# Optimization experiments

Measured on AMD Instinct MI355X. Metric: run time of the kernel, lower is better.

## Reference

```python
import jax, jax.numpy as jnp
import numpy as np

B, NB, H, E, NCT, NL = 16, 4096, 128, 65536, 32, 2
LN_EPS = 1e-5


def _layernorm(x, scale, bias):
    mu = jnp.mean(x, axis=-1, keepdims=True)
    var = jnp.var(x, axis=-1, keepdims=True)
    return (x - mu) / jnp.sqrt(var + LN_EPS) * scale + bias


def setup_inputs() -> dict:
    key = jax.random.key(0)
    ks = jax.random.split(key, 18)
    s = 1.0 / np.sqrt(H)
    inp = {
        'block_tokens': jax.random.normal(ks[0], (B, NB, H), jnp.float32),
        'edge_structure': jnp.full((E,), 0.5, jnp.float32),
        'ct_emb': 0.1 * jax.random.normal(ks[1], (NCT, E), jnp.float32),
        'W_proj': s * jax.random.normal(ks[2], (H, H), jnp.float32),
        'b_proj': jnp.zeros((H,), jnp.float32),
        'W_gate': (1.0 / np.sqrt(2 * H)) * jax.random.normal(ks[3], (2 * H, H), jnp.float32),
        'b_gate': jnp.zeros((H,), jnp.float32),
        'ln_scale': jnp.ones((NL, H), jnp.float32),
        'ln_bias': jnp.zeros((NL, H), jnp.float32),
        'W1': s * jax.random.normal(ks[4], (NL, H, 2 * H), jnp.float32),
        'b1': jnp.zeros((NL, 2 * H), jnp.float32),
        'W2': (1.0 / np.sqrt(2 * H)) * jax.random.normal(ks[5], (NL, 2 * H, H), jnp.float32),
        'b2': jnp.zeros((NL, H), jnp.float32),
        'cancer_type': jax.random.randint(ks[6], (B,), 0, NCT),
        'edge_src': jax.random.randint(ks[7], (E,), 0, NB),
        'edge_dst': jax.random.randint(ks[8], (E,), 0, NB),
        'block_active': jax.random.bernoulli(ks[9], 0.9, (B, NB)),
    }
    return inp


def reference(block_tokens, edge_structure, ct_emb, W_proj, b_proj, W_gate, b_gate,
              ln_scale, ln_bias, W1, b1, W2, b2,
              cancer_type, edge_src, edge_dst, block_active):
    # per-edge signed weights, masked by active src/dst blocks  -> (B, E)
    structure = jax.nn.sigmoid(edge_structure)
    edge_w = structure[None, :] * ct_emb[cancer_type]
    edge_w = edge_w * block_active[:, edge_src].astype(edge_w.dtype) \
                    * block_active[:, edge_dst].astype(edge_w.dtype)
    # route projection + ELU
    h_route = jax.nn.elu(jnp.einsum('bnh,hd->bnd', block_tokens, W_proj) + b_proj)
    # gather sources, weight, scatter-add to destinations
    weighted = edge_w[..., None] * h_route[:, edge_src, :]          # (B, E, H)
    messages = jnp.zeros_like(block_tokens).at[:, edge_dst, :].add(weighted)
    # gated residual
    gate = jax.nn.sigmoid(
        jnp.einsum('bnh,hd->bnd', jnp.concatenate([block_tokens, messages], axis=-1), W_gate) + b_gate)
    x = block_tokens + gate * messages
    # norm + FFN layers (dropout is identity at inference)
    for l in range(NL):
        normed = _layernorm(x, ln_scale[l], ln_bias[l])
        h = jax.nn.elu(jnp.einsum('bnh,hf->bnf', normed, W1[l]) + b1[l])
        x = x + jnp.einsum('bnf,fh->bnh', h, W2[l]) + b2[l]
    return (x, edge_w)
```

## Files before the change

kernel.cpp:

```cpp
#include <hip/hip_runtime.h>
#include <hip/hip_bf16.h>

#define BB     16
#define NBLK   4096
#define HD     128
#define NE     65536
#define MTOT   (BB * NBLK)

typedef __attribute__((ext_vector_type(8))) short bf16x8;
typedef __attribute__((ext_vector_type(4))) float f32x4;

__device__ __forceinline__ float bf2f(unsigned short u) {
    union { unsigned int i; float f; } v; v.i = ((unsigned int)u) << 16; return v.f;
}
__device__ __forceinline__ unsigned short f2bf(float f) {
    union { float f; unsigned int i; } v; v.f = f;
    unsigned int u = v.i;
    unsigned int r = u + 0x7FFFu + ((u >> 16) & 1u);
    return (unsigned short)(r >> 16);
}
__device__ __forceinline__ float ldf(const void* p, size_t i, int f32m) {
    return f32m ? ((const float*)p)[i] : bf2f(((const unsigned short*)p)[i]);
}
__device__ __forceinline__ int get_active(const void* p, int i, int mode) {
    switch (mode) {
        case 1:  return ((const unsigned char*)p)[i] != 0;
        case 2:  return ((const unsigned short*)p)[i] != 0;
        case 3:  return ((const float*)p)[i] != 0.f;
        default: return ((const int*)p)[i] != 0;
    }
}
__device__ __forceinline__ float elu_f(float v) {
    const float e = __expf(v);
    return v > 0.f ? v : e - 1.f;
}
__device__ __forceinline__ float sig_f(float v) {
    return 1.f / (1.f + __expf(-v));
}

__global__ void probe_k(const unsigned int* __restrict__ es,
                        const unsigned int* __restrict__ act,
                        int* __restrict__ flags)
{
    const int lane = threadIdx.x;
    const unsigned int v0 = act[lane], v1 = act[64 + lane];
    auto le1  = [](unsigned int v) { return v <= 1u; };
    auto byt  = [](unsigned int v) {
        return ((v & 0xFFu) <= 1u) && (((v >> 8) & 0xFFu) <= 1u) &&
               (((v >> 16) & 0xFFu) <= 1u) && ((v >> 24) <= 1u); };
    auto f32b = [](unsigned int v) { return v == 0u || v == 0x3F800000u; };
    auto bfb  = [](unsigned int v) {
        unsigned short h0 = (unsigned short)(v & 0xFFFFu), h1 = (unsigned short)(v >> 16);
        return (h0 == 0u || h0 == 0x3F80u) && (h1 == 0u || h1 == 0x3F80u); };
    const unsigned long long m_le1 = __ballot(le1(v0) && le1(v1));
    const unsigned long long m_byt = __ballot(byt(v0) && byt(v1));
    const unsigned long long m_f32 = __ballot(f32b(v0) && f32b(v1));
    const unsigned long long m_bf  = __ballot(bfb(v0) && bfb(v1));
    if (lane == 0) {
        flags[0] = (es[0] != 0x3F003F00u) ? 1 : 0;
        const unsigned long long full = ~0ull;
        flags[1] = (m_le1 == full) ? 0
                 : (m_byt == full) ? 1
                 : (m_f32 == full) ? 3
                 : (m_bf  == full) ? 2 : 0;
    }
}

__global__ __launch_bounds__(256) void cvt_k(const void* __restrict__ bt,
                                             unsigned short* __restrict__ bt16,
                                             const int* __restrict__ flags)
{
    const size_t i = ((size_t)blockIdx.x * 256 + threadIdx.x) * 8;
    if (flags[0]) {
        const float* q = (const float*)bt + i;
        f32x4 lo = *(const f32x4*)q;
        f32x4 hi = *(const f32x4*)(q + 4);
        bf16x8 r;
        #pragma unroll
        for (int j = 0; j < 4; ++j) { r[j] = (short)f2bf(lo[j]); r[4 + j] = (short)f2bf(hi[j]); }
        *(bf16x8*)(bt16 + i) = r;
    } else {
        *(bf16x8*)(bt16 + i) = *(const bf16x8*)((const unsigned short*)bt + i);
    }
}

__global__ __launch_bounds__(256) void transpose_k(
    const void* p0, const void* p1, const void* p2, const void* p3,
    const void* p4, const void* p5, unsigned short* __restrict__ wsT,
    const int* __restrict__ flags)
{
    const void* srcs[6]  = {p0, p1, p2, p3, p4, p5};
    const int eoffs[6]   = {0, 0, 0, 32768, 0, 32768};
    const int Ks[6]      = {128, 256, 128, 128, 256, 256};
    const int nsh[6]     = {7,   7,   8,   8,   7,   7};
    const int offs[6]    = {0, 16384, 49152, 81920, 114688, 147456};
    const int f32m = flags[0];
    const int z = blockIdx.y;
    const int K = Ks[z];
    const int Nn = 1 << nsh[z];
    const int idx = blockIdx.x * 256 + threadIdx.x;
    if (idx >= K * Nn) return;
    const int k = idx >> nsh[z];
    const int n = idx & (Nn - 1);
    wsT[offs[z] + n * K + k] = f2bf(ldf(srcs[z], (size_t)eoffs[z] + idx, f32m));
}

__global__ __launch_bounds__(256) void csr_count_k(const int* __restrict__ edst,
                                                   int* __restrict__ cnt)
{
    const int e = blockIdx.x * 256 + threadIdx.x;
    atomicAdd(&cnt[edst[e]], 1);
}

__global__ __launch_bounds__(1024) void csr_scan_k(const int* __restrict__ cnt,
                                                   int* __restrict__ ofs,
                                                   int* __restrict__ cur)
{
    __shared__ int part[1024];
    const int t = threadIdx.x;
    const int4 c = ((const int4*)cnt)[t];
    part[t] = c.x + c.y + c.z + c.w;
    __syncthreads();
    #pragma unroll
    for (int off = 1; off < 1024; off <<= 1) {
        const int v = (t >= off) ? part[t - off] : 0;
        __syncthreads();
        part[t] += v;
        __syncthreads();
    }
    const int base = t ? part[t - 1] : 0;
    int4 o;
    o.x = base; o.y = o.x + c.x; o.z = o.y + c.y; o.w = o.z + c.z;
    ((int4*)ofs)[t] = o;
    ((int4*)cur)[t] = o;
    if (t == 1023) ofs[4096] = part[1023];
}

__global__ __launch_bounds__(256) void csr_fill_k(const int* __restrict__ edst,
                                                  int* __restrict__ cur,
                                                  int* __restrict__ eidx,
                                                  int* __restrict__ pos_e)
{
    const int e = blockIdx.x * 256 + threadIdx.x;
    const int pos = atomicAdd(&cur[edst[e]], 1);
    eidx[pos] = e;
    pos_e[e] = pos;
}

__global__ __launch_bounds__(256) void edge_k(
    const void* __restrict__ es, const void* __restrict__ ctE,
    const int* __restrict__ ctype, const int* __restrict__ esrc, const int* __restrict__ edst,
    const void* __restrict__ act, const int* __restrict__ pos_e,
    float* __restrict__ out_ew, float2* __restrict__ compact,
    const int* __restrict__ flags)
{
    const int f32m = flags[0], am = flags[1];
    const int idx = blockIdx.x * 256 + threadIdx.x;
    const int b = idx >> 16;
    const int e = idx & 65535;
    const int s = esrc[e];
    const float sv  = sig_f(ldf(es, e, f32m));
    const float emb = ldf(ctE, (size_t)ctype[b] * NE + e, f32m);
    const int a1 = get_active(act, b * NBLK + s, am);
    const int a2 = get_active(act, b * NBLK + edst[e], am);
    const float w = (a1 && a2) ? sv * emb : 0.f;
    out_ew[idx] = w;
    compact[((size_t)b << 16) + pos_e[e]] = make_float2(w, __int_as_float(s));
}

__global__ __launch_bounds__(256) void gather_k(
    const float2* __restrict__ compact, const int* __restrict__ ofs,
    const unsigned short* __restrict__ hr, unsigned short* __restrict__ msg)
{
    const int blk = blockIdx.x;
    const int xcd = blk & 7;
    const int i   = blk >> 3;
    const int b   = xcd * 2 + (i & 1);
    const int d   = ((i >> 1) << 2) | (threadIdx.x >> 6);
    const int lane = threadIdx.x & 63;
    const int sub  = lane >> 4;
    const int l15  = lane & 15;
    const int j1 = ofs[d + 1];
    const size_t bbase = (size_t)b * NBLK * HD;
    const float2* cb = compact + ((size_t)b << 16);
    float acc[8];
    #pragma unroll
    for (int i2 = 0; i2 < 8; ++i2) acc[i2] = 0.f;
    int j = ofs[d] + sub;
    float2 c = (j < j1) ? cb[j] : make_float2(0.f, 0.f);
    while (j < j1) {
        const int jn = j + 4;
        const float2 cn = (jn < j1) ? cb[jn] : make_float2(0.f, 0.f);
        if (c.x != 0.f) {
            const int src = __float_as_int(c.y);
            const bf16x8 v = *(const bf16x8*)(hr + bbase + (size_t)src * HD + l15 * 8);
            #pragma unroll
            for (int i2 = 0; i2 < 8; ++i2)
                acc[i2] += c.x * bf2f((unsigned short)v[i2]);
        }
        c = cn; j = jn;
    }
    #pragma unroll
    for (int i2 = 0; i2 < 8; ++i2) {
        acc[i2] += __shfl_xor(acc[i2], 16);
        acc[i2] += __shfl_xor(acc[i2], 32);
    }
    if (sub == 0) {
        bf16x8 o;
        #pragma unroll
        for (int i2 = 0; i2 < 8; ++i2) o[i2] = (short)f2bf(acc[i2]);
        *(bf16x8*)(msg + bbase + (size_t)d * HD + l15 * 8) = o;
    }
}

template<int K, int N, int EPI>
__global__ __launch_bounds__(256) void gemm_k(
    const unsigned short* __restrict__ A,
    const unsigned short* __restrict__ WT,
    const void* __restrict__ bias, long boff,
    unsigned short* __restrict__ outb,
    const int* __restrict__ flags)
{
    constexpr int KI    = K / 32;
    constexpr int NCW   = N / 4;
    constexpr int NTW   = NCW / 16;
    constexpr int TILES = 4;
    constexpr int NBUF  = (K == 128 ? 4 : 2);
    const int f32m = flags[0];
    const int t    = threadIdx.x;
    const int lane = t & 63;
    const int wave = t >> 6;
    const int q    = lane >> 4;
    const int l15  = lane & 15;
    const int n0   = wave * NCW;

    bf16x8 Bf[KI][NTW];
    #pragma unroll
    for (int ki = 0; ki < KI; ++ki)
        #pragma unroll
        for (int nt = 0; nt < NTW; ++nt)
            Bf[ki][nt] = *(const bf16x8*)(WT + (size_t)(n0 + nt * 16 + l15) * K + ki * 32 + q * 8);

    float biasv[NTW];
    #pragma unroll
    for (int nt = 0; nt < NTW; ++nt)
        biasv[nt] = ldf(bias, boff + n0 + nt * 16 + l15, f32m);

    const int tile0 = blockIdx.x * TILES;
    bf16x8 Af[NBUF][KI];
    auto loadA = [&](int tt) {
        const int arow = (tile0 + tt) * 16 + l15;
        #pragma unroll
        for (int ki = 0; ki < KI; ++ki)
            Af[tt % NBUF][ki] = *(const bf16x8*)(A + (size_t)arow * K + ki * 32 + q * 8);
    };
    #pragma unroll
    for (int p = 0; p < NBUF; ++p) loadA(p);

    #pragma unroll
    for (int tt = 0; tt < TILES; ++tt) {
        const int s = tt % NBUF;
        f32x4 acc[NTW];
        #pragma unroll
        for (int i = 0; i < NTW; ++i) acc[i] = (f32x4){0.f, 0.f, 0.f, 0.f};
        #pragma unroll
        for (int ki = 0; ki < KI; ++ki)
            #pragma unroll
            for (int nt = 0; nt < NTW; ++nt)
                acc[nt] = __builtin_amdgcn_mfma_f32_16x16x32_bf16(Af[s][ki], Bf[ki][nt], acc[nt], 0, 0, 0);

        if (tt + NBUF < TILES) loadA(tt + NBUF);

        const int m0 = (tile0 + tt) * 16;
        #pragma unroll
        for (int nt = 0; nt < NTW; ++nt) {
            #pragma unroll
            for (int r = 0; r < 4; ++r) {
                const int row = m0 + q * 4 + r;
                const int col = n0 + nt * 16 + l15;
                const float v = acc[nt][r] + biasv[nt];
                outb[(size_t)row * N + col] = f2bf(elu_f(v));
            }
        }
    }
}

__global__ __launch_bounds__(256) void mega_k(
    const unsigned short* __restrict__ bt16,
    const unsigned short* __restrict__ msg,
    const void* __restrict__ btf,
    const unsigned short* __restrict__ WT,
    const void* __restrict__ bg,
    const void* __restrict__ b1, const void* __restrict__ b2,
    const void* __restrict__ lns, const void* __restrict__ lnb,
    float* __restrict__ xout,
    const int* __restrict__ flags)
{
    constexpr int R = 32;
    __shared__ __align__(16) float          x_lds[R][132];
    __shared__ __align__(16) unsigned short nrm_lds[R][136];
    __shared__ __align__(16) unsigned short h_lds[R][264];

    const int f32m = flags[0];
    const int t    = threadIdx.x;
    const int lane = t & 63;
    const int wave = t >> 6;
    const int q    = lane >> 4;
    const int l15  = lane & 15;
    const int row0 = blockIdx.x * R;

    const int ng = wave * 32;
    const unsigned short* WgT = WT + 16384;

    bf16x8 Bg[8][2];
    #pragma unroll
    for (int ki = 0; ki < 8; ++ki)
        #pragma unroll
        for (int nt = 0; nt < 2; ++nt)
            Bg[ki][nt] = *(const bf16x8*)(WgT + (size_t)(ng + nt * 16 + l15) * 256 + ki * 32 + q * 8);
    float biasg[2];
    #pragma unroll
    for (int nt = 0; nt < 2; ++nt) biasg[nt] = ldf(bg, ng + nt * 16 + l15, f32m);

    bf16x8 Ag[2][8];
    #pragma unroll
    for (int tt = 0; tt < 2; ++tt) {
        const int arow = row0 + tt * 16 + l15;
        #pragma unroll
        for (int ki = 0; ki < 8; ++ki) {
            const int k = ki * 32 + q * 8;
            Ag[tt][ki] = (k < HD)
                ? *(const bf16x8*)(bt16 + (size_t)arow * HD + k)
                : *(const bf16x8*)(msg  + (size_t)arow * HD + (k - HD));
        }
    }

    float btv[2][2][4], mgv[2][2][4];
    #pragma unroll
    for (int tt = 0; tt < 2; ++tt)
        #pragma unroll
        for (int nt = 0; nt < 2; ++nt)
            #pragma unroll
            for (int r = 0; r < 4; ++r) {
                const size_t gi = (size_t)(row0 + tt * 16 + q * 4 + r) * HD + ng + nt * 16 + l15;
                btv[tt][nt][r] = ldf(btf, gi, f32m);
                mgv[tt][nt][r] = bf2f(msg[gi]);
            }

    #pragma unroll
    for (int tt = 0; tt < 2; ++tt) {
        f32x4 acc[2];
        #pragma unroll
        for (int nt = 0; nt < 2; ++nt) acc[nt] = (f32x4){0.f, 0.f, 0.f, 0.f};
        #pragma unroll
        for (int ki = 0; ki < 8; ++ki)
            #pragma unroll
            for (int nt = 0; nt < 2; ++nt)
                acc[nt] = __builtin_amdgcn_mfma_f32_16x16x32_bf16(Ag[tt][ki], Bg[ki][nt], acc[nt], 0, 0, 0);
        #pragma unroll
        for (int nt = 0; nt < 2; ++nt)
            #pragma unroll
            for (int r = 0; r < 4; ++r) {
                const float g = sig_f(acc[nt][r] + biasg[nt]);
                x_lds[tt * 16 + q * 4 + r][ng + nt * 16 + l15] =
                    btv[tt][nt][r] + g * mgv[tt][nt][r];
            }
    }
    __syncthreads();

    const int rowln = t >> 3;
    const int seg   = t & 7;
    const int n1 = wave * 64;
    const int n2 = wave * 32;

    #pragma unroll
    for (int l = 0; l < 2; ++l) {
        const unsigned short* W1T = WT + (l ? 81920  : 49152);
        const unsigned short* W2T = WT + (l ? 147456 : 114688);
        const long b1o = l ? 256 : 0, b2o = l ? 128 : 0, lno = l ? 128 : 0;

        bf16x8 B1[4][4];
        #pragma unroll
        for (int ki = 0; ki < 4; ++ki)
            #pragma unroll
            for (int nt = 0; nt < 4; ++nt)
                B1[ki][nt] = *(const bf16x8*)(W1T + (size_t)(n1 + nt * 16 + l15) * 128 + ki * 32 + q * 8);
        float bias1[4];
        #pragma unroll
        for (int nt = 0; nt < 4; ++nt) bias1[nt] = ldf(b1, b1o + n1 + nt * 16 + l15, f32m);

        f32x4 xv[4];
        #pragma unroll
        for (int j = 0; j < 4; ++j) xv[j] = *(const f32x4*)&x_lds[rowln][seg * 16 + j * 4];
        float s = 0.f, ss = 0.f;
        #pragma unroll
        for (int j = 0; j < 4; ++j)
            #pragma unroll
            for (int k = 0; k < 4; ++k) { const float v = xv[j][k]; s += v; ss += v * v; }
        #pragma unroll
        for (int off = 1; off < 8; off <<= 1) { s += __shfl_xor(s, off); ss += __shfl_xor(ss, off); }
        const float mu = s * (1.f / 128.f);
        const float rs = rsqrtf(ss * (1.f / 128.f) - mu * mu + 1e-5f);
        bf16x8 nv[2];
        #pragma unroll
        for (int j = 0; j < 4; ++j)
            #pragma unroll
            for (int k = 0; k < 4; ++k) {
                const int col = seg * 16 + j * 4 + k;
                const float nn = (xv[j][k] - mu) * rs * ldf(lns, lno + col, f32m)
                                 + ldf(lnb, lno + col, f32m);
                nv[j >> 1][(j & 1) * 4 + k] = (short)f2bf(nn);
            }
        *(bf16x8*)&nrm_lds[rowln][seg * 16]     = nv[0];
        *(bf16x8*)&nrm_lds[rowln][seg * 16 + 8] = nv[1];
        __syncthreads();

        #pragma unroll
        for (int tt = 0; tt < 2; ++tt) {
            bf16x8 Af[4];
            #pragma unroll
            for (int ki = 0; ki < 4; ++ki)
                Af[ki] = *(const bf16x8*)&nrm_lds[tt * 16 + l15][ki * 32 + q * 8];
            f32x4 acc[4];
            #pragma unroll
            for (int nt = 0; nt < 4; ++nt) acc[nt] = (f32x4){0.f, 0.f, 0.f, 0.f};
            #pragma unroll
            for (int ki = 0; ki < 4; ++ki)
                #pragma unroll
                for (int nt = 0; nt < 4; ++nt)
                    acc[nt] = __builtin_amdgcn_mfma_f32_16x16x32_bf16(Af[ki], B1[ki][nt], acc[nt], 0, 0, 0);
            #pragma unroll
            for (int nt = 0; nt < 4; ++nt)
                #pragma unroll
                for (int r = 0; r < 4; ++r)
                    h_lds[tt * 16 + q * 4 + r][n1 + nt * 16 + l15] =
                        f2bf(elu_f(acc[nt][r] + bias1[nt]));
        }

        bf16x8 B2[8][2];
        #pragma unroll
        for (int ki = 0; ki < 8; ++ki)
            #pragma unroll
            for (int nt = 0; nt < 2; ++nt)
                B2[ki][nt] = *(const bf16x8*)(W2T + (size_t)(n2 + nt * 16 + l15) * 256 + ki * 32 + q * 8);
        float bias2[2];
        #pragma unroll
        for (int nt = 0; nt < 2; ++nt) bias2[nt] = ldf(b2, b2o + n2 + nt * 16 + l15, f32m);
        __syncthreads();

        #pragma unroll
        for (int tt = 0; tt < 2; ++tt) {
            bf16x8 Ah[8];
            #pragma unroll
            for (int ki = 0; ki < 8; ++ki)
                Ah[ki] = *(const bf16x8*)&h_lds[tt * 16 + l15][ki * 32 + q * 8];
            f32x4 acc[2];
            #pragma unroll
            for (int nt = 0; nt < 2; ++nt) acc[nt] = (f32x4){0.f, 0.f, 0.f, 0.f};
            #pragma unroll
            for (int ki = 0; ki < 8; ++ki)
                #pragma unroll
                for (int nt = 0; nt < 2; ++nt)
                    acc[nt] = __builtin_amdgcn_mfma_f32_16x16x32_bf16(Ah[ki], B2[ki][nt], acc[nt], 0, 0, 0);
            #pragma unroll
            for (int nt = 0; nt < 2; ++nt)
                #pragma unroll
                for (int r = 0; r < 4; ++r)
                    x_lds[tt * 16 + q * 4 + r][n2 + nt * 16 + l15] += acc[nt][r] + bias2[nt];
        }
        __syncthreads();
    }

    float* xo = xout + (size_t)row0 * HD;
    #pragma unroll
    for (int j = 0; j < 4; ++j) {
        const int idx = j * 256 + t;
        const int r2  = idx >> 5;
        const int c4  = (idx & 31) * 4;
        *(f32x4*)(xo + (size_t)idx * 4) = *(const f32x4*)&x_lds[r2][c4];
    }
}

extern "C" void kernel_launch(void* const* d_in, const int* in_sizes, int n_in,
                              void* d_out, int out_size, void* d_ws, size_t ws_size,
                              hipStream_t stream)
{
    (void)in_sizes; (void)n_in; (void)out_size; (void)ws_size;

    const void* bt  = d_in[0];
    const void* es  = d_in[1];
    const void* ctE = d_in[2];
    const void* Wp  = d_in[3];
    const void* bp  = d_in[4];
    const void* Wg  = d_in[5];
    const void* bg  = d_in[6];
    const void* lns = d_in[7];
    const void* lnb = d_in[8];
    const void* W1  = d_in[9];
    const void* b1  = d_in[10];
    const void* W2  = d_in[11];
    const void* b2  = d_in[12];
    const int* ctype = (const int*)d_in[13];
    const int* esrc  = (const int*)d_in[14];
    const int* edst  = (const int*)d_in[15];
    const void* act  = d_in[16];

    float* out_x  = (float*)d_out;
    float* out_ew = out_x + (size_t)MTOT * HD;
    float* x = out_x;

    char* ws = (char*)d_ws;
    int*            flags = (int*)ws;
    unsigned short* msg   = (unsigned short*)(ws + 1024);
    unsigned short* bt16  = (unsigned short*)(ws + 1024 + (16ull << 20));
    unsigned short* hr    = (unsigned short*)(ws + 1024 + (32ull << 20));
    char* base48 = ws + 1024 + (48ull << 20);
    int*            cnt     = (int*)(base48);
    int*            ofs     = (int*)(base48 + (16 << 10));
    int*            cur     = (int*)(base48 + (36 << 10));
    int*            eidx    = (int*)(base48 + (52 << 10));
    int*            pos_e   = (int*)(base48 + (308 << 10));
    unsigned short* WT      = (unsigned short*)(base48 + (576 << 10));
    float2*         compact = (float2*)(base48 + (1 << 20));

    const int M = MTOT;

    probe_k<<<1, 64, 0, stream>>>((const unsigned int*)es, (const unsigned int*)act, flags);
    hipMemsetAsync(cnt, 0, NBLK * sizeof(int), stream);

    cvt_k<<<dim3((M * HD / 8) / 256), 256, 0, stream>>>(bt, bt16, flags);
    transpose_k<<<dim3(128, 6), 256, 0, stream>>>(Wp, Wg, W1, W1, W2, W2, WT, flags);

    csr_count_k<<<dim3(NE / 256), 256, 0, stream>>>(edst, cnt);
    csr_scan_k<<<dim3(1), 1024, 0, stream>>>(cnt, ofs, cur);
    csr_fill_k<<<dim3(NE / 256), 256, 0, stream>>>(edst, cur, eidx, pos_e);

    edge_k<<<dim3((BB * NE) / 256), 256, 0, stream>>>(
        es, ctE, ctype, esrc, edst, act, pos_e, out_ew, compact, flags);

    gemm_k<128, 128, 0><<<dim3(M / 64), 256, 0, stream>>>(
        bt16, WT + 0, bp, 0, hr, flags);

    gather_k<<<dim3(M / 4), 256, 0, stream>>>(compact, ofs, hr, msg);

    mega_k<<<dim3(M / 32), 256, 0, stream>>>(
        bt16, msg, bt, WT, bg, b1, b2, lns, lnb, x, flags);
}
```

Before: 327.7 us.

## Restructure fused gate+FFN kernel so each wave owns 16 rows independently

The fused gate/layernorm/FFN kernel now gives each wave its own 16-row tile and computes all output columns for it, keeping the residual x in registers and using a small per-wave LDS scratch instead of block-shared x/norm/h buffers. This removes all __syncthreads barriers and the cross-wave LDS traffic for x. Each block handles 64 rows instead of 32, so the grid is halved. Weights are now streamed from global/L2 per nt iteration instead of being held per wave, which increases weight load traffic per row tile and register pressure from the xreg array.

```diff
diff --git a/kernel.cpp b/kernel.cpp
--- a/kernel.cpp
+++ b/kernel.cpp
@@ -296,10 +296,7 @@
     float* __restrict__ xout,
     const int* __restrict__ flags)
 {
-    constexpr int R = 32;
-    __shared__ __align__(16) float          x_lds[R][132];
-    __shared__ __align__(16) unsigned short nrm_lds[R][136];
-    __shared__ __align__(16) unsigned short h_lds[R][264];
+    __shared__ __align__(16) unsigned short scr_all[4][16][264];
 
     const int f32m = flags[0];
     const int t    = threadIdx.x;
@@ -307,177 +304,136 @@
     const int wave = t >> 6;
     const int q    = lane >> 4;
     const int l15  = lane & 15;
-    const int row0 = blockIdx.x * R;
-
-    const int ng = wave * 32;
+    const int r0   = (blockIdx.x * 4 + wave) * 16;
+
+    unsigned short (* __restrict__ S)[264] = scr_all[wave];
+
     const unsigned short* WgT = WT + 16384;
 
-    bf16x8 Bg[8][2];
-    #pragma unroll
-    for (int ki = 0; ki < 8; ++ki)
-        #pragma unroll
-        for (int nt = 0; nt < 2; ++nt)
-            Bg[ki][nt] = *(const bf16x8*)(WgT + (size_t)(ng + nt * 16 + l15) * 256 + ki * 32 + q * 8);
-    float biasg[2];
-    #pragma unroll
-    for (int nt = 0; nt < 2; ++nt) biasg[nt] = ldf(bg, ng + nt * 16 + l15, f32m);
-
-    bf16x8 Ag[2][8];
-    #pragma unroll
-    for (int tt = 0; tt < 2; ++tt) {
-        const int arow = row0 + tt * 16 + l15;
+    bf16x8 Ag[8];
+    #pragma unroll
+    for (int ki = 0; ki < 8; ++ki) {
+        const int k = ki * 32 + q * 8;
+        Ag[ki] = (k < HD)
+            ? *(const bf16x8*)(bt16 + (size_t)(r0 + l15) * HD + k)
+            : *(const bf16x8*)(msg  + (size_t)(r0 + l15) * HD + (k - HD));
+    }
+    float xreg[8][4];
+    #pragma unroll
+    for (int nt = 0; nt < 8; ++nt)
+        #pragma unroll
+        for (int r = 0; r < 4; ++r)
+            xreg[nt][r] = ldf(btf, (size_t)(r0 + q * 4 + r) * HD + nt * 16 + l15, f32m);
+
+    #pragma unroll
+    for (int nt = 0; nt < 8; ++nt) {
+        const int col = nt * 16 + l15;
+        f32x4 acc = (f32x4){0.f, 0.f, 0.f, 0.f};
         #pragma unroll
         for (int ki = 0; ki < 8; ++ki) {
-            const int k = ki * 32 + q * 8;
-            Ag[tt][ki] = (k < HD)
-                ? *(const bf16x8*)(bt16 + (size_t)arow * HD + k)
-                : *(const bf16x8*)(msg  + (size_t)arow * HD + (k - HD));
-        }
-    }
-
-    float btv[2][2][4], mgv[2][2][4];
-    #pragma unroll
-    for (int tt = 0; tt < 2; ++tt)
-        #pragma unroll
-        for (int nt = 0; nt < 2; ++nt)
-            #pragma unroll
-            for (int r = 0; r < 4; ++r) {
-                const size_t gi = (size_t)(row0 + tt * 16 + q * 4 + r) * HD + ng + nt * 16 + l15;
-                btv[tt][nt][r] = ldf(btf, gi, f32m);
-                mgv[tt][nt][r] = bf2f(msg[gi]);
-            }
-
-    #pragma unroll
-    for (int tt = 0; tt < 2; ++tt) {
-        f32x4 acc[2];
-        #pragma unroll
-        for (int nt = 0; nt < 2; ++nt) acc[nt] = (f32x4){0.f, 0.f, 0.f, 0.f};
-        #pragma unroll
-        for (int ki = 0; ki < 8; ++ki)
-            #pragma unroll
-            for (int nt = 0; nt < 2; ++nt)
-                acc[nt] = __builtin_amdgcn_mfma_f32_16x16x32_bf16(Ag[tt][ki], Bg[ki][nt], acc[nt], 0, 0, 0);
-        #pragma unroll
-        for (int nt = 0; nt < 2; ++nt)
-            #pragma unroll
-            for (int r = 0; r < 4; ++r) {
-                const float g = sig_f(acc[nt][r] + biasg[nt]);
-                x_lds[tt * 16 + q * 4 + r][ng + nt * 16 + l15] =
-                    btv[tt][nt][r] + g * mgv[tt][nt][r];
-            }
-    }
-    __syncthreads();
-
-    const int rowln = t >> 3;
-    const int seg   = t & 7;
-    const int n1 = wave * 64;
-    const int n2 = wave * 32;
+            const bf16x8 Bg = *(const bf16x8*)(WgT + (size_t)col * 256 + ki * 32 + q * 8);
+            acc = __builtin_amdgcn_mfma_f32_16x16x32_bf16(Ag[ki], Bg, acc, 0, 0, 0);
+        }
+        const float bgv = ldf(bg, col, f32m);
+        #pragma unroll
+        for (int r = 0; r < 4; ++r) {
+            const float mg = bf2f(msg[(size_t)(r0 + q * 4 + r) * HD + col]);
+            xreg[nt][r] += sig_f(acc[r] + bgv) * mg;
+        }
+    }
 
     #pragma unroll
     for (int l = 0; l < 2; ++l) {
         const unsigned short* W1T = WT + (l ? 81920  : 49152);
         const unsigned short* W2T = WT + (l ? 147456 : 114688);
-        const long b1o = l ? 256 : 0, b2o = l ? 128 : 0, lno = l ? 128 : 0;
-
-        bf16x8 B1[4][4];
+        const int b1o = l ? 256 : 0, b2o = l ? 128 : 0, lno = l ? 128 : 0;
+
+        float s[4], ss[4];
+        #pragma unroll
+        for (int r = 0; r < 4; ++r) { s[r] = 0.f; ss[r] = 0.f; }
+        #pragma unroll
+        for (int nt = 0; nt < 8; ++nt)
+            #pragma unroll
+            for (int r = 0; r < 4; ++r) { const float v = xreg[nt][r]; s[r] += v; ss[r] += v * v; }
+        #pragma unroll
+        for (int off = 1; off < 16; off <<= 1)
+            #pragma unroll
+            for (int r = 0; r < 4; ++r) {
+                s[r]  += __shfl_xor(s[r],  off);
+                ss[r] += __shfl_xor(ss[r], off);
+            }
+        float mu[4], rs[4];
+        #pragma unroll
+        for (int r = 0; r < 4; ++r) {
+            mu[r] = s[r] * (1.f / 128.f);
+            rs[r] = rsqrtf(ss[r] * (1.f / 128.f) - mu[r] * mu[r] + 1e-5f);
+        }
+
+        #pragma unroll
+        for (int nt = 0; nt < 8; ++nt) {
+            const int col = nt * 16 + l15;
+            const float scv = ldf(lns, lno + col, f32m);
+            const float biv = ldf(lnb, lno + col, f32m);
+            #pragma unroll
+            for (int r = 0; r < 4; ++r)
+                S[q * 4 + r][col] = f2bf((xreg[nt][r] - mu[r]) * rs[r] * scv + biv);
+        }
+
+        bf16x8 An[4];
         #pragma unroll
         for (int ki = 0; ki < 4; ++ki)
-            #pragma unroll
-            for (int nt = 0; nt < 4; ++nt)
-                B1[ki][nt] = *(const bf16x8*)(W1T + (size_t)(n1 + nt * 16 + l15) * 128 + ki * 32 + q * 8);
-        float bias1[4];
-        #pragma unroll
-        for (int nt = 0; nt < 4; ++nt) bias1[nt] = ldf(b1, b1o + n1 + nt * 16 + l15, f32m);
-
-        f32x4 xv[4];
-        #pragma unroll
-        for (int j = 0; j < 4; ++j) xv[j] = *(const f32x4*)&x_lds[rowln][seg * 16 + j * 4];
-        float s = 0.f, ss = 0.f;
-        #pragma unroll
-        for (int j = 0; j < 4; ++j)
-            #pragma unroll
-            for (int k = 0; k < 4; ++k) { const float v = xv[j][k]; s += v; ss += v * v; }
-        #pragma unroll
-        for (int off = 1; off < 8; off <<= 1) { s += __shfl_xor(s, off); ss += __shfl_xor(ss, off); }
-        const float mu = s * (1.f / 128.f);
-        const float rs = rsqrtf(ss * (1.f / 128.f) - mu * mu + 1e-5f);
-        bf16x8 nv[2];
-        #pragma unroll
-        for (int j = 0; j < 4; ++j)
-            #pragma unroll
-            for (int k = 0; k < 4; ++k) {
-                const int col = seg * 16 + j * 4 + k;
-                const float nn = (xv[j][k] - mu) * rs * ldf(lns, lno + col, f32m)
-                                 + ldf(lnb, lno + col, f32m);
-                nv[j >> 1][(j & 1) * 4 + k] = (short)f2bf(nn);
+            An[ki] = *(const bf16x8*)&S[l15][ki * 32 + q * 8];
+
+        #pragma unroll 4
+        for (int nt = 0; nt < 16; ++nt) {
+            const int col = nt * 16 + l15;
+            f32x4 acc = (f32x4){0.f, 0.f, 0.f, 0.f};
+            #pragma unroll
+            for (int ki = 0; ki < 4; ++ki) {
+                const bf16x8 B1 = *(const bf16x8*)(W1T + (size_t)col * 128 + ki * 32 + q * 8);
+                acc = __builtin_amdgcn_mfma_f32_16x16x32_bf16(An[ki], B1, acc, 0, 0, 0);
             }
-        *(bf16x8*)&nrm_lds[rowln][seg * 16]     = nv[0];
-        *(bf16x8*)&nrm_lds[rowln][seg * 16 + 8] = nv[1];
-        __syncthreads();
-
-        #pragma unroll
-        for (int tt = 0; tt < 2; ++tt) {
-            bf16x8 Af[4];
-            #pragma unroll
-            for (int ki = 0; ki < 4; ++ki)
-                Af[ki] = *(const bf16x8*)&nrm_lds[tt * 16 + l15][ki * 32 + q * 8];
-            f32x4 acc[4];
-            #pragma unroll
-            for (int nt = 0; nt < 4; ++nt) acc[nt] = (f32x4){0.f, 0.f, 0.f, 0.f};
-            #pragma unroll
-            for (int ki = 0; ki < 4; ++ki)
-                #pragma unroll
-                for (int nt = 0; nt < 4; ++nt)
-                    acc[nt] = __builtin_amdgcn_mfma_f32_16x16x32_bf16(Af[ki], B1[ki][nt], acc[nt], 0, 0, 0);
-            #pragma unroll
-            for (int nt = 0; nt < 4; ++nt)
-                #pragma unroll
-                for (int r = 0; r < 4; ++r)
-                    h_lds[tt * 16 + q * 4 + r][n1 + nt * 16 + l15] =
-                        f2bf(elu_f(acc[nt][r] + bias1[nt]));
-        }
-
-        bf16x8 B2[8][2];
+            const float b1v = ldf(b1, b1o + col, f32m);
+            #pragma unroll
+            for (int r = 0; r < 4; ++r)
+                S[q * 4 + r][col] = f2bf(elu_f(acc[r] + b1v));
+        }
+
+        bf16x8 Ah[8];
         #pragma unroll
         for (int ki = 0; ki < 8; ++ki)
-            #pragma unroll
-            for (int nt = 0; nt < 2; ++nt)
-                B2[ki][nt] = *(const bf16x8*)(W2T + (size_t)(n2 + nt * 16 + l15) * 256 + ki * 32 + q * 8);
-        float bias2[2];
-        #pragma unroll
-        for (int nt = 0; nt < 2; ++nt) bias2[nt] = ldf(b2, b2o + n2 + nt * 16 + l15, f32m);
-        __syncthreads();
-
-        #pragma unroll
-        for (int tt = 0; tt < 2; ++tt) {
-            bf16x8 Ah[8];
-            #pragma unroll
-            for (int ki = 0; ki < 8; ++ki)
-                Ah[ki] = *(const bf16x8*)&h_lds[tt * 16 + l15][ki * 32 + q * 8];
-            f32x4 acc[2];
-            #pragma unroll
-            for (int nt = 0; nt < 2; ++nt) acc[nt] = (f32x4){0.f, 0.f, 0.f, 0.f};
-            #pragma unroll
-            for (int ki = 0; ki < 8; ++ki)
-                #pragma unroll
-                for (int nt = 0; nt < 2; ++nt)
-                    acc[nt] = __builtin_amdgcn_mfma_f32_16x16x32_bf16(Ah[ki], B2[ki][nt], acc[nt], 0, 0, 0);
-            #pragma unroll
-            for (int nt = 0; nt < 2; ++nt)
-                #pragma unroll
-                for (int r = 0; r < 4; ++r)
-                    x_lds[tt * 16 + q * 4 + r][n2 + nt * 16 + l15] += acc[nt][r] + bias2[nt];
-        }
-        __syncthreads();
-    }
-
-    float* xo = xout + (size_t)row0 * HD;
-    #pragma unroll
-    for (int j = 0; j < 4; ++j) {
-        const int idx = j * 256 + t;
-        const int r2  = idx >> 5;
+            Ah[ki] = *(const bf16x8*)&S[l15][ki * 32 + q * 8];
+
+        #pragma unroll
+        for (int nt = 0; nt < 8; ++nt) {
+            const int col = nt * 16 + l15;
+            f32x4 acc = (f32x4){0.f, 0.f, 0.f, 0.f};
+            #pragma unroll
+            for (int ki = 0; ki < 8; ++ki) {
+                const bf16x8 B2 = *(const bf16x8*)(W2T + (size_t)col * 256 + ki * 32 + q * 8);
+                acc = __builtin_amdgcn_mfma_f32_16x16x32_bf16(Ah[ki], B2, acc, 0, 0, 0);
+            }
+            const float b2v = ldf(b2, b2o + col, f32m);
+            #pragma unroll
+            for (int r = 0; r < 4; ++r)
+                xreg[nt][r] += acc[r] + b2v;
+        }
+    }
+
+    float* __restrict__ F = (float*)&S[0][0];
+    #pragma unroll
+    for (int nt = 0; nt < 8; ++nt)
+        #pragma unroll
+        for (int r = 0; r < 4; ++r)
+            F[(q * 4 + r) * 132 + nt * 16 + l15] = xreg[nt][r];
+
+    float* xo = xout + (size_t)r0 * HD;
+    #pragma unroll
+    for (int j = 0; j < 8; ++j) {
+        const int idx = j * 64 + lane;
+        const int rr  = idx >> 5;
         const int c4  = (idx & 31) * 4;
-        *(f32x4*)(xo + (size_t)idx * 4) = *(const f32x4*)&x_lds[r2][c4];
+        *(f32x4*)(xo + (size_t)idx * 4) = *(const f32x4*)&F[rr * 132 + c4];
     }
 }
 
@@ -543,6 +499,6 @@
 
     gather_k<<<dim3(M / 4), 256, 0, stream>>>(compact, ofs, hr, msg);
 
-    mega_k<<<dim3(M / 32), 256, 0, stream>>>(
+    mega_k<<<dim3(M / 64), 256, 0, stream>>>(
         bt16, msg, bt, WT, bg, b1, b2, lns, lnb, x, flags);
 }
```

New measurement: 355.8 us. +8.6%, slower.
